# Optimization experiments

Measured on AMD Instinct MI355X. Metric: run time of the kernel, lower is better.

Reference implementation:

```python
import jax, jax.numpy as jnp
import numpy as np

HEADS = 16


def fenwick_mask(T):
    # Boolean [T, T] mask: diagonal + Fenwick-tree lookback positions, causal.
    m = np.zeros((T, T), dtype=bool)
    for i in range(T):
        j = i + 1
        while j <= T:
            m[i, j - 1] = True
            j += j & -j
        step = 1
        while i - step >= 0:
            m[i, i - step] = True
            step *= 2
    m &= np.tril(np.ones((T, T), dtype=bool))  # causal
    return jnp.asarray(m)


def setup_inputs() -> dict:
    key = jax.random.key(0)
    ks = jax.random.split(key, 4)
    B, T, C = 2, 2048, 1024
    x = jax.random.normal(ks[0], (B, T, C), dtype=jnp.float32)
    W_qkv = jax.random.normal(ks[1], (C, 3 * C), dtype=jnp.float32) * (C ** -0.5)
    b_qkv = jnp.zeros((3 * C,), dtype=jnp.float32)
    W_proj = jax.random.normal(ks[2], (C, C), dtype=jnp.float32) * (C ** -0.5)
    b_proj = jnp.zeros((C,), dtype=jnp.float32)
    return {"x": x, "W_qkv": W_qkv, "b_qkv": b_qkv, "W_proj": W_proj, "b_proj": b_proj}


def reference(x, W_qkv, b_qkv, W_proj, b_proj):
    B, T, C = x.shape
    H = HEADS
    Dh = C // H
    scale = Dh ** -0.5
    qkv = (x @ W_qkv + b_qkv).reshape(B, T, 3, H, Dh)
    qkv = jnp.transpose(qkv, (2, 0, 3, 1, 4))  # [3, B, H, T, Dh]
    q, k, v = qkv[0], qkv[1], qkv[2]
    attn = jnp.einsum('bhtd,bhsd->bhts', q, k) * scale  # [B, H, T, T]
    mask = fenwick_mask(T)  # trace-time constant
    attn = jnp.where(mask[None, None], attn, -jnp.inf)
    attn = jax.nn.softmax(attn, axis=-1)
    out = jnp.einsum('bhts,bhsd->bhtd', attn, v)  # [B, H, T, Dh]
    out = jnp.transpose(out, (0, 2, 1, 3)).reshape(B, T, C)
    return out @ W_proj + b_proj
```

## Files before the change

### kernel.cpp

```cpp
#include <hip/hip_runtime.h>
#include <hip/hip_bf16.h>


typedef unsigned short ushort_t;
typedef __attribute__((ext_vector_type(8))) short s16x8;
typedef __attribute__((ext_vector_type(4))) float f32x4;

#define T_SEQ 2048
#define C_DIM 1024
#define HEADS 16

__device__ __forceinline__ ushort_t f2bf(float f) {
    union { float f; unsigned u; } v{f};
    unsigned r = v.u + 0x7FFFu + ((v.u >> 16) & 1u);
    return (ushort_t)(r >> 16);
}
__device__ __forceinline__ float bf2f(ushort_t u) {
    union { unsigned u; float f; } v{((unsigned)u) << 16};
    return v.f;
}

__device__ __forceinline__ void async16(const ushort_t* g, ushort_t* l) {
    __builtin_amdgcn_global_load_lds(
        (const __attribute__((address_space(1))) void*)g,
        (__attribute__((address_space(3))) void*)l, 16, 0, 0);
}

__global__ void prep(const float* __restrict__ x, ushort_t* __restrict__ xb,
                     const float* __restrict__ Wq, ushort_t* __restrict__ WqT,
                     const float* __restrict__ Wp, ushort_t* __restrict__ WpT) {
    const int bid = blockIdx.x;
    const int tid = threadIdx.x;
    if (bid < 4096) {
        const int i = bid * 256 + tid;
        float4 f = ((const float4*)x)[i];
        ushort4 o;
        o.x = f2bf(f.x); o.y = f2bf(f.y); o.z = f2bf(f.z); o.w = f2bf(f.w);
        ((ushort4*)xb)[i] = o;
    } else {
        __shared__ ushort_t tile[32][33];
        const float* W; ushort_t* WT; int N, nb, kb;
        if (bid < 7168) {
            const int tb = bid - 4096;
            W = Wq; WT = WqT; N = 3072; nb = (tb % 96) * 32; kb = (tb / 96) * 32;
        } else {
            const int tb = bid - 7168;
            W = Wp; WT = WpT; N = 1024; nb = (tb & 31) * 32; kb = (tb >> 5) * 32;
        }
        const int tx = tid & 31, ty = tid >> 5;
        #pragma unroll
        for (int i = ty; i < 32; i += 8)
            tile[i][tx] = f2bf(W[(size_t)(kb + i) * N + nb + tx]);
        __syncthreads();
        #pragma unroll
        for (int i = ty; i < 32; i += 8)
            WT[(size_t)(nb + i) * 1024 + kb + tx] = tile[tx][i];
    }
}

#define BAR()  do { __builtin_amdgcn_sched_barrier(0); __builtin_amdgcn_s_barrier(); \
                    __builtin_amdgcn_sched_barrier(0); } while (0)
#define WAIT_LGKM0() do { asm volatile("s_waitcnt lgkmcnt(0)" ::: "memory"); \
                          __builtin_amdgcn_sched_barrier(0); } while (0)
#define WAIT_VM(n)  asm volatile("s_waitcnt vmcnt(" #n ")" ::: "memory")

#define SA(kt, u, dst) async16(Ag + (size_t)(u) * rstep + (size_t)(kt) * 64, \
                               (dst) + (u) * 4096 + wave * 512)
#define SB(kt, u, dst) async16(Bg + (size_t)(u) * rstep + (size_t)(kt) * 64, \
                               (dst) + (u) * 4096 + wave * 512)

#define LDA_FRAG(buf, i, kh) (*(const s16x8*)((buf) + ((wm << 7) + (i) * 16 + lrow) * 64 \
                               + ((((kh) * 4 + quad) ^ d3) << 3)))
#define LDB_FRAG(buf, j, kh) (*(const s16x8*)((buf) + (wn * 48 + (j) * 16 + lrow) * 64 \
                               + ((((kh) * 4 + quad) ^ d3) << 3)))

#define PHASE2(lAb, lBb, F0, LOADB, STAGES, ENDWAIT)                            \
  {                                                                             \
    s16x8 af[4][2];                                                             \
    _Pragma("unroll") for (int ii = 0; ii < 4; ++ii)                            \
      _Pragma("unroll") for (int kh = 0; kh < 2; ++kh)                          \
        af[ii][kh] = LDA_FRAG(lAb, (F0) + ii, kh);                              \
    if (LOADB) {                                                                \
      _Pragma("unroll") for (int j = 0; j < 3; ++j)                             \
        _Pragma("unroll") for (int kh = 0; kh < 2; ++kh)                        \
          bf[j][kh] = LDB_FRAG(lBb, j, kh);                                     \
    }                                                                           \
    STAGES;                                                                     \
    BAR();                                                                      \
    WAIT_LGKM0();                                                               \
    __builtin_amdgcn_s_setprio(1);                                              \
    _Pragma("unroll") for (int ii = 0; ii < 4; ++ii)                            \
      _Pragma("unroll") for (int j = 0; j < 3; ++j)                             \
        _Pragma("unroll") for (int kh = 0; kh < 2; ++kh)                        \
          acc[(F0) + ii][j] = __builtin_amdgcn_mfma_f32_16x16x32_bf16(          \
              af[ii][kh], bf[j][kh], acc[(F0) + ii][j], 0, 0, 0);               \
    __builtin_amdgcn_s_setprio(0);                                              \
    ENDWAIT;                                                                    \
    BAR();                                                                      \
  }

__global__ __launch_bounds__(512, 2)
void gemm_qkv(const ushort_t* __restrict__ A, const ushort_t* __restrict__ BT,
              const float* __restrict__ bias, ushort_t* __restrict__ C,
              int N, int K) {
    __shared__ ushort_t lds[57344];

    const int tid  = threadIdx.x;
    const int wave = tid >> 6;
    const int lane = tid & 63;
    const int wm   = wave >> 2;
    const int wn   = wave & 3;
    const int lrow = lane & 15;
    const int quad = lane >> 4;
    const int d3   = lrow & 7;
    const int crow = lane >> 3;
    const int gcol = (((lane & 7) ^ crow) << 3);

    const int bid    = blockIdx.x;
    const int xcd    = bid & 7;
    const int q      = bid >> 3;
    const int rowblk = ((xcd & 3) << 2) + (q & 3);
    const int colblk = ((xcd >> 2) << 3) + (q >> 2);
    const int row0   = rowblk * 256;
    const int col0   = colblk * 192;

    ushort_t* const lA0 = lds;
    ushort_t* const lB0 = lds + 16384;
    ushort_t* const lA1 = lds + 28672;
    ushort_t* const lB1 = lds + 45056;

    const ushort_t* Ag = A  + (size_t)(row0 + wave * 8 + crow) * K + gcol;
    const ushort_t* Bg = BT + (size_t)(col0 + wave * 8 + crow) * K + gcol;
    const size_t rstep = (size_t)64 * K;

    f32x4 acc[8][3] = {};
    s16x8 bf[3][2];

    SA(0, 0, lA0); SA(0, 1, lA0); SA(0, 2, lA0); SA(0, 3, lA0);
    SB(0, 0, lB0); SB(0, 1, lB0); SB(0, 2, lB0);
    SB(1, 0, lB1); SB(1, 1, lB1); SB(1, 2, lB1); SA(1, 0, lA1); SA(1, 2, lA1);
    WAIT_VM(5);
    BAR();

    const int nt = K >> 6;
    for (int t = 0; t < nt; t += 2) {
        const bool s2 = (t + 2) < nt;
        PHASE2(lA0, lB0, 0, true, { SA(t + 1, 1, lA1); SA(t + 1, 3, lA1); }, {});
        PHASE2(lA0, lB0, 4, false,
               { if (s2) { SB(t + 2, 0, lB0); SB(t + 2, 1, lB0); SB(t + 2, 2, lB0);
                           SA(t + 2, 0, lA0); SA(t + 2, 2, lA0); } },
               { if (s2) { WAIT_VM(5); } else { WAIT_VM(0); } });
        PHASE2(lA1, lB1, 0, true, { if (s2) { SA(t + 2, 1, lA0); SA(t + 2, 3, lA0); } }, {});
        PHASE2(lA1, lB1, 4, false,
               { if (s2) { SB(t + 3, 0, lB1); SB(t + 3, 1, lB1); SB(t + 3, 2, lB1);
                           SA(t + 3, 0, lA1); SA(t + 3, 2, lA1); } },
               { if (s2) { WAIT_VM(5); } });
    }

    #pragma unroll
    for (int i = 0; i < 8; ++i) {
        #pragma unroll
        for (int j = 0; j < 3; ++j) {
            const int col = col0 + wn * 48 + j * 16 + lrow;
            const float bv = bias[col];
            #pragma unroll
            for (int r = 0; r < 4; ++r) {
                const int row = row0 + (wm << 7) + i * 16 + quad * 4 + r;
                C[(size_t)row * N + col] = f2bf(acc[i][j][r] + bv);
            }
        }
    }
}

__global__ void gemm_proj(const ushort_t* __restrict__ A, const ushort_t* __restrict__ BT,
                          const float* __restrict__ bias, float* __restrict__ C,
                          int N, int K) {
    __shared__ ushort_t lsA[128 * 64];
    __shared__ ushort_t lsB[128 * 64];

    const int tid  = threadIdx.x;
    const int wave = tid >> 6;
    const int lane = tid & 63;

    const int bid  = blockIdx.x;
    const int xcd  = bid & 7;
    const int q    = bid >> 3;
    const int row0 = (xcd * 4 + (q & 3)) * 128;
    const int col0 = (q >> 2) * 128;

    const int wr   = (wave >> 1) * 64;
    const int wc   = (wave & 1) * 64;
    const int lrow = lane & 15;
    const int quad = lane >> 4;
    const int crow = lane >> 3;
    const int gcol = ((lane & 7) ^ crow) * 8;
    const int d3   = lrow & 7;

    f32x4 acc[4][4] = {};

    for (int k0 = 0; k0 < K; k0 += 64) {
        #pragma unroll
        for (int it = 0; it < 4; ++it) {
            const int chunk = it * 4 + wave;
            const int r = chunk * 8 + crow;
            async16(A  + (size_t)(row0 + r) * K + (k0 + gcol), lsA + chunk * 512);
            async16(BT + (size_t)(col0 + r) * K + (k0 + gcol), lsB + chunk * 512);
        }
        __syncthreads();
        #pragma unroll
        for (int kk = 0; kk < 64; kk += 32) {
            const int g = (kk >> 3) + quad;
            const int slot = (g ^ d3) << 3;
            s16x8 af[4], bfr[4];
            #pragma unroll
            for (int i = 0; i < 4; ++i)
                af[i] = *(const s16x8*)(lsA + (wr + i * 16 + lrow) * 64 + slot);
            #pragma unroll
            for (int j = 0; j < 4; ++j)
                bfr[j] = *(const s16x8*)(lsB + (wc + j * 16 + lrow) * 64 + slot);
            #pragma unroll
            for (int i = 0; i < 4; ++i)
                #pragma unroll
                for (int j = 0; j < 4; ++j)
                    acc[i][j] = __builtin_amdgcn_mfma_f32_16x16x32_bf16(
                        af[i], bfr[j], acc[i][j], 0, 0, 0);
        }
        __syncthreads();
    }

    #pragma unroll
    for (int i = 0; i < 4; ++i) {
        #pragma unroll
        for (int j = 0; j < 4; ++j) {
            const int col = col0 + wc + j * 16 + lrow;
            const float bv = bias[col];
            #pragma unroll
            for (int r = 0; r < 4; ++r) {
                const int row = row0 + wr + i * 16 + quad * 4 + r;
                C[(size_t)row * N + col] = acc[i][j][r] + bv;
            }
        }
    }
}

__global__ void fenwick_attn(const ushort_t* __restrict__ QKV, ushort_t* __restrict__ AO) {
    const int lane = threadIdx.x & 63;
    const int bid  = blockIdx.x;
    const int xcd  = bid & 7;
    const int q    = bid >> 3;
    const int bh   = xcd + ((q >> 6) << 3);
    const int tile = ((q & 63) << 2) + (threadIdx.x >> 6);
    const int h    = bh & (HEADS - 1);
    const int b    = bh >> 4;
    const int tl   = lane >> 3;
    const int g    = lane & 7;
    const int t    = tile * 8 + tl;

    const ushort_t* base = QKV + (size_t)(b * T_SEQ) * 3072 + h * 64 + g * 8;

    float qf[8];
    {
        s16x8 qv = *(const s16x8*)(base + (size_t)t * 3072);
        #pragma unroll
        for (int e = 0; e < 8; ++e) qf[e] = bf2f((ushort_t)qv[e]);
    }

    float logit[12];
    int   pos[12];
    float mx = -1e30f;
    #pragma unroll
    for (int s = 0; s < 12; ++s) {
        const int step = (s == 0) ? 0 : (1 << (s - 1));
        const bool act = (step <= t);
        const int p = act ? (t - step) : t;
        pos[s] = p;
        s16x8 kv = *(const s16x8*)(base + (size_t)p * 3072 + 1024);
        float l = 0.f;
        #pragma unroll
        for (int e = 0; e < 8; ++e) l = fmaf(qf[e], bf2f((ushort_t)kv[e]), l);
        l += __shfl_xor(l, 1, 64);
        l += __shfl_xor(l, 2, 64);
        l += __shfl_xor(l, 4, 64);
        l *= 0.125f;
        logit[s] = act ? l : -1e30f;
        mx = fmaxf(mx, logit[s]);
    }

    float denom = 0.f;
    float ov[8] = {};
    #pragma unroll
    for (int s = 0; s < 12; ++s) {
        const float w = __expf(logit[s] - mx);
        denom += w;
        s16x8 vv = *(const s16x8*)(base + (size_t)pos[s] * 3072 + 2048);
        #pragma unroll
        for (int e = 0; e < 8; ++e) ov[e] = fmaf(w, bf2f((ushort_t)vv[e]), ov[e]);
    }

    const float inv = 1.f / denom;
    s16x8 os;
    #pragma unroll
    for (int e = 0; e < 8; ++e) os[e] = (short)f2bf(ov[e] * inv);
    *(s16x8*)(AO + (size_t)(b * T_SEQ + t) * C_DIM + h * 64 + g * 8) = os;
}

extern "C" void kernel_launch(void* const* d_in, const int* in_sizes, int n_in,
                              void* d_out, int out_size, void* d_ws, size_t ws_size,
                              hipStream_t stream) {
    const float* x      = (const float*)d_in[0];
    const float* W_qkv  = (const float*)d_in[1];
    const float* b_qkv  = (const float*)d_in[2];
    const float* W_proj = (const float*)d_in[3];
    const float* b_proj = (const float*)d_in[4];
    float* out = (float*)d_out;

    char* ws = (char*)d_ws;
    ushort_t* xb     = (ushort_t*)(ws);
    ushort_t* WqkvT  = (ushort_t*)(ws + (size_t)8  * 1048576);
    ushort_t* QKVb   = (ushort_t*)(ws + (size_t)14 * 1048576);
    ushort_t* AO     = (ushort_t*)(ws + (size_t)38 * 1048576);
    ushort_t* WprojT = (ushort_t*)(ws + (size_t)46 * 1048576);

    prep<<<8192, 256, 0, stream>>>(x, xb, W_qkv, WqkvT, W_proj, WprojT);
    gemm_qkv<<<256, 512, 0, stream>>>(xb, WqkvT, b_qkv, QKVb, 3072, 1024);
    fenwick_attn<<<2048, 256, 0, stream>>>(QKVb, AO);
    gemm_proj<<<256, 256, 0, stream>>>(AO, WprojT, b_proj, out, 1024, 1024);
}
```

Baseline: 147.5 us.

## Drop per-phase trailing barrier in QKV GEMM and double-buffer projection GEMM

In the QKV GEMM, each phase now has a single barrier instead of two. The global-load wait moves ahead of that barrier, and the scheduling fences around it are removed. The projection GEMM gains a two-stage LDS double buffer, so the next K tile is prefetched asynchronously while MFMAs run on the current one. The goal is to cut barrier stalls and hide global-memory latency, at the cost of double the LDS for the projection kernel and a higher risk of LDS read/write races in the QKV kernel now that the post-compute barrier is gone.

```diff
diff --git a/kernel.cpp b/kernel.cpp
--- a/kernel.cpp
+++ b/kernel.cpp
@@ -58,8 +58,6 @@
     }
 }
 
-#define BAR()  do { __builtin_amdgcn_sched_barrier(0); __builtin_amdgcn_s_barrier(); \
-                    __builtin_amdgcn_sched_barrier(0); } while (0)
 #define WAIT_LGKM0() do { asm volatile("s_waitcnt lgkmcnt(0)" ::: "memory"); \
                           __builtin_amdgcn_sched_barrier(0); } while (0)
 #define WAIT_VM(n)  asm volatile("s_waitcnt vmcnt(" #n ")" ::: "memory")
@@ -74,7 +72,7 @@
 #define LDB_FRAG(buf, j, kh) (*(const s16x8*)((buf) + (wn * 48 + (j) * 16 + lrow) * 64 \
                                + ((((kh) * 4 + quad) ^ d3) << 3)))
 
-#define PHASE2(lAb, lBb, F0, LOADB, STAGES, ENDWAIT)                            \
+#define PHASE3(lAb, lBb, F0, LOADB, STAGES, PREBAR)                             \
   {                                                                             \
     s16x8 af[4][2];                                                             \
     _Pragma("unroll") for (int ii = 0; ii < 4; ++ii)                            \
@@ -86,7 +84,8 @@
           bf[j][kh] = LDB_FRAG(lBb, j, kh);                                     \
     }                                                                           \
     STAGES;                                                                     \
-    BAR();                                                                      \
+    PREBAR;                                                                     \
+    __builtin_amdgcn_s_barrier();                                               \
     WAIT_LGKM0();                                                               \
     __builtin_amdgcn_s_setprio(1);                                              \
     _Pragma("unroll") for (int ii = 0; ii < 4; ++ii)                            \
@@ -95,8 +94,6 @@
           acc[(F0) + ii][j] = __builtin_amdgcn_mfma_f32_16x16x32_bf16(          \
               af[ii][kh], bf[j][kh], acc[(F0) + ii][j], 0, 0, 0);               \
     __builtin_amdgcn_s_setprio(0);                                              \
-    ENDWAIT;                                                                    \
-    BAR();                                                                      \
   }
 
 __global__ __launch_bounds__(512, 2)
@@ -140,18 +137,18 @@
     SB(0, 0, lB0); SB(0, 1, lB0); SB(0, 2, lB0);
     SB(1, 0, lB1); SB(1, 1, lB1); SB(1, 2, lB1); SA(1, 0, lA1); SA(1, 2, lA1);
     WAIT_VM(5);
-    BAR();
+    __builtin_amdgcn_s_barrier();
 
     const int nt = K >> 6;
     for (int t = 0; t < nt; t += 2) {
         const bool s2 = (t + 2) < nt;
-        PHASE2(lA0, lB0, 0, true, { SA(t + 1, 1, lA1); SA(t + 1, 3, lA1); }, {});
-        PHASE2(lA0, lB0, 4, false,
+        PHASE3(lA0, lB0, 0, true, { SA(t + 1, 1, lA1); SA(t + 1, 3, lA1); }, {});
+        PHASE3(lA0, lB0, 4, false,
                { if (s2) { SB(t + 2, 0, lB0); SB(t + 2, 1, lB0); SB(t + 2, 2, lB0);
                            SA(t + 2, 0, lA0); SA(t + 2, 2, lA0); } },
                { if (s2) { WAIT_VM(5); } else { WAIT_VM(0); } });
-        PHASE2(lA1, lB1, 0, true, { if (s2) { SA(t + 2, 1, lA0); SA(t + 2, 3, lA0); } }, {});
-        PHASE2(lA1, lB1, 4, false,
+        PHASE3(lA1, lB1, 0, true, { if (s2) { SA(t + 2, 1, lA0); SA(t + 2, 3, lA0); } }, {});
+        PHASE3(lA1, lB1, 4, false,
                { if (s2) { SB(t + 3, 0, lB1); SB(t + 3, 1, lB1); SB(t + 3, 2, lB1);
                            SA(t + 3, 0, lA1); SA(t + 3, 2, lA1); } },
                { if (s2) { WAIT_VM(5); } });
@@ -172,11 +169,20 @@
     }
 }
 
+#define PSTAGE(t, b) do {                                                        \
+    _Pragma("unroll") for (int it = 0; it < 4; ++it) {                           \
+        const int chunk = it * 4 + wave;                                         \
+        const int r = chunk * 8 + crow;                                          \
+        async16(A  + (size_t)(row0 + r) * K + ((t) * 64 + gcol), lsA[b] + chunk * 512); \
+        async16(BT + (size_t)(col0 + r) * K + ((t) * 64 + gcol), lsB[b] + chunk * 512); \
+    }                                                                            \
+} while (0)
+
 __global__ void gemm_proj(const ushort_t* __restrict__ A, const ushort_t* __restrict__ BT,
                           const float* __restrict__ bias, float* __restrict__ C,
                           int N, int K) {
-    __shared__ ushort_t lsA[128 * 64];
-    __shared__ ushort_t lsB[128 * 64];
+    __shared__ ushort_t lsA[2][128 * 64];
+    __shared__ ushort_t lsB[2][128 * 64];
 
     const int tid  = threadIdx.x;
     const int wave = tid >> 6;
@@ -198,15 +204,12 @@
 
     f32x4 acc[4][4] = {};
 
-    for (int k0 = 0; k0 < K; k0 += 64) {
-        #pragma unroll
-        for (int it = 0; it < 4; ++it) {
-            const int chunk = it * 4 + wave;
-            const int r = chunk * 8 + crow;
-            async16(A  + (size_t)(row0 + r) * K + (k0 + gcol), lsA + chunk * 512);
-            async16(BT + (size_t)(col0 + r) * K + (k0 + gcol), lsB + chunk * 512);
-        }
-        __syncthreads();
+    const int nt = K >> 6;
+    int cur = 0;
+    PSTAGE(0, 0);
+    __syncthreads();
+    for (int t = 0; t < nt; ++t) {
+        if (t + 1 < nt) PSTAGE(t + 1, cur ^ 1);
         #pragma unroll
         for (int kk = 0; kk < 64; kk += 32) {
             const int g = (kk >> 3) + quad;
@@ -214,10 +217,10 @@
             s16x8 af[4], bfr[4];
             #pragma unroll
             for (int i = 0; i < 4; ++i)
-                af[i] = *(const s16x8*)(lsA + (wr + i * 16 + lrow) * 64 + slot);
+                af[i] = *(const s16x8*)(lsA[cur] + (wr + i * 16 + lrow) * 64 + slot);
             #pragma unroll
             for (int j = 0; j < 4; ++j)
-                bfr[j] = *(const s16x8*)(lsB + (wc + j * 16 + lrow) * 64 + slot);
+                bfr[j] = *(const s16x8*)(lsB[cur] + (wc + j * 16 + lrow) * 64 + slot);
             #pragma unroll
             for (int i = 0; i < 4; ++i)
                 #pragma unroll
@@ -226,6 +229,7 @@
                         af[i], bfr[j], acc[i][j], 0, 0, 0);
         }
         __syncthreads();
+        cur ^= 1;
     }
 
     #pragma unroll
```

After: 145.0 us (median of 2 runs). Within noise of the previous version (-1.7%).
